# Kernel optimization log

Measured on AMD Instinct MI355X. Metric: run time of the kernel, lower is better.

Reference implementation:

```python
import jax, jax.numpy as jnp
import numpy as np

DIM, HID, E, K = 1024, 2048, 8, 2


def setup_inputs() -> dict:
    key = jax.random.key(0)
    ks = jax.random.split(key, 5)
    x = jax.random.normal(ks[0], (2, 2048, DIM), dtype=jnp.float32)
    # router (torch zero-inits; use small random so routing is non-degenerate)
    router_w = jax.random.normal(ks[1], (DIM, E), dtype=jnp.float32) * 0.02
    router_b = jnp.zeros((E,), dtype=jnp.float32)
    # stacked expert params: w12 [E, dim, 2*hidden], w3 [E, hidden, dim]
    w12 = jax.random.normal(ks[2], (E, DIM, 2 * HID), dtype=jnp.float32) * 0.02
    w3 = jax.random.normal(ks[3], (E, HID, DIM), dtype=jnp.float32) * 0.02
    return {"x": x, "router_w": router_w, "router_b": router_b, "w12": w12, "w3": w3}


def reference(x, router_w, router_b, w12, w3):
    # router logits [b, s, e]; eval mode -> no jitter noise
    logits = jnp.einsum("bsd,de->bse", x, router_w) + router_b
    scores = jax.nn.sigmoid(logits)
    top_v, top_i = jax.lax.top_k(scores, K)            # [b, s, k]
    rw = top_v / (jnp.sum(top_v, axis=-1, keepdims=True) + 1e-6)
    # per-token combine weight for each expert (0 if not routed)
    oh = jax.nn.one_hot(top_i, E, dtype=x.dtype)       # [b, s, k, e]
    cw = jnp.einsum("bsk,bske->bse", rw, oh)           # [b, s, e]
    # dense all-expert SwiGLU (matches original masked-dense math)
    x12 = jnp.einsum("bsd,edh->bseh", x, w12)          # [b, s, e, 2H]
    x1, x2 = jnp.split(x12, 2, axis=-1)
    h = jax.nn.silu(x1) * x2                           # [b, s, e, H]
    eout = jnp.einsum("bseh,ehd->bsed", h, w3)         # [b, s, e, dim]
    out = jnp.einsum("bsed,bse->bsd", eout, cw)
    aux_loss = 0.01 * jnp.mean(logits ** 2)
    return out, aux_loss
```

## Files before the change

kernel.cpp:

```cpp
#include <hip/hip_runtime.h>
#include <hip/hip_bf16.h>
#include <stdint.h>

typedef __bf16 bf16_t;
typedef __bf16 bf16x8 __attribute__((ext_vector_type(8)));
typedef __bf16 bf16x4 __attribute__((ext_vector_type(4)));
typedef float f32x4 __attribute__((ext_vector_type(4)));

#define T_TOK 4096
#define DIM   1024
#define HID   2048
#define NE    8
#define MAXT  72

__device__ __forceinline__ void gload_lds16(const void* g, void* l) {
  __builtin_amdgcn_global_load_lds(
      (const __attribute__((address_space(1))) unsigned int*)g,
      (__attribute__((address_space(3))) unsigned int*)l, 16, 0, 0);
}

__global__ __launch_bounds__(256) void k_wt(const float* __restrict__ in,
                                            bf16_t* __restrict__ out,
                                            int K, int N) {
  __shared__ float tile[128][65];
  const size_t eoff = (size_t)blockIdx.z * K * N;
  const int k0 = blockIdx.y * 128, n0 = blockIdx.x * 64;
  const int tid = threadIdx.x;
#pragma unroll
  for (int it = 0; it < 8; ++it) {
    int k = (tid >> 4) + it * 16;
    int n = (tid & 15) * 4;
    float4 v = *(const float4*)(in + eoff + (size_t)(k0 + k) * N + n0 + n);
    tile[k][n] = v.x; tile[k][n + 1] = v.y; tile[k][n + 2] = v.z; tile[k][n + 3] = v.w;
  }
  __syncthreads();
#pragma unroll
  for (int it = 0; it < 4; ++it) {
    int n = (tid >> 4) + it * 16;
    int kc = (tid & 15) * 8;
    bf16x8 o;
#pragma unroll
    for (int j = 0; j < 8; ++j) o[j] = (bf16_t)tile[kc + j][n];
    *(bf16x8*)(out + eoff + (size_t)(n0 + n) * K + k0 + kc) = o;
  }
}

__global__ __launch_bounds__(256) void k_router(const float* __restrict__ x,
    const float* __restrict__ rw, const float* __restrict__ rb,
    int* __restrict__ counts, int* __restrict__ top_i, float* __restrict__ top_w,
    float* __restrict__ aux, bf16_t* __restrict__ xb) {
  int t = blockIdx.x * 4 + (threadIdx.x >> 6);
  int lane = threadIdx.x & 63;
  const float* xt = x + (size_t)t * DIM;
  float acc[8] = {0.f,0.f,0.f,0.f,0.f,0.f,0.f,0.f};
#pragma unroll
  for (int it = 0; it < 4; ++it) {
    int i = (it * 64 + lane) * 4;
    float4 xv = *(const float4*)(xt + i);
    bf16x4 o;
    o[0] = (bf16_t)xv.x; o[1] = (bf16_t)xv.y; o[2] = (bf16_t)xv.z; o[3] = (bf16_t)xv.w;
    *(bf16x4*)(xb + (size_t)t * DIM + i) = o;
#pragma unroll
    for (int c = 0; c < 4; ++c) {
      float v = (c == 0) ? xv.x : (c == 1) ? xv.y : (c == 2) ? xv.z : xv.w;
      float4 r0 = *(const float4*)(rw + (size_t)(i + c) * 8);
      float4 r1 = *(const float4*)(rw + (size_t)(i + c) * 8 + 4);
      acc[0] += v * r0.x; acc[1] += v * r0.y; acc[2] += v * r0.z; acc[3] += v * r0.w;
      acc[4] += v * r1.x; acc[5] += v * r1.y; acc[6] += v * r1.z; acc[7] += v * r1.w;
    }
  }
#pragma unroll
  for (int m = 32; m >= 1; m >>= 1) {
#pragma unroll
    for (int e = 0; e < 8; ++e) acc[e] += __shfl_xor(acc[e], m, 64);
  }
  if (lane == 0) {
    float s[8]; float sumsq = 0.f;
#pragma unroll
    for (int e = 0; e < 8; ++e) {
      float lg = acc[e] + rb[e];
      sumsq += lg * lg;
      s[e] = 1.f / (1.f + __expf(-lg));
    }
    int i1 = 0;
#pragma unroll
    for (int e = 1; e < 8; ++e) if (s[e] > s[i1]) i1 = e;
    int i2 = (i1 == 0) ? 1 : 0;
#pragma unroll
    for (int e = 0; e < 8; ++e) if (e != i1 && s[e] > s[i2]) i2 = e;
    float v1 = s[i1], v2 = s[i2];
    float den = v1 + v2 + 1e-6f;
    top_i[2 * t]     = i1; top_i[2 * t + 1] = i2;
    top_w[2 * t]     = v1 / den;
    top_w[2 * t + 1] = v2 / den;
    atomicAdd(&counts[i1], 1);
    atomicAdd(&counts[i2], 1);
    atomicAdd(aux, 0.01f * sumsq * (1.f / 32768.f));
  }
}

__global__ void k_plan(const int* __restrict__ counts, int* __restrict__ base,
                       int* __restrict__ tile_e, int* __restrict__ tile_m0) {
  if (threadIdx.x == 0) {
    int s = 0, nt = 0;
    for (int e = 0; e < NE; ++e) {
      base[e] = s;
      int c = counts[e];
      for (int m0 = 0; m0 < c; m0 += 128) { tile_e[nt] = e; tile_m0[nt] = m0; ++nt; }
      s += c;
    }
    for (; nt < MAXT; ++nt) tile_e[nt] = -1;
  }
}

__global__ __launch_bounds__(256) void k_gather(const int* __restrict__ top_i,
    const float* __restrict__ top_w, const int* __restrict__ base,
    int* __restrict__ fill, int* __restrict__ slot_token, float* __restrict__ slot_wt,
    int* __restrict__ slot_of) {
  int t = blockIdx.x * 256 + threadIdx.x;
  if (t >= T_TOK) return;
#pragma unroll
  for (int j = 0; j < 2; ++j) {
    int e = top_i[2 * t + j];
    int p = atomicAdd(&fill[e], 1);
    int g = base[e] + p;
    slot_token[g] = t;
    slot_wt[g]    = top_w[2 * t + j];
    slot_of[2 * t + j] = g;
  }
}

__global__ __launch_bounds__(256) void k_gemm1(
    const bf16_t* __restrict__ xb, const bf16_t* __restrict__ w12t,
    const int* __restrict__ counts, const int* __restrict__ base,
    const int* __restrict__ tile_e, const int* __restrict__ tile_m0,
    const int* __restrict__ slot_token, bf16_t* __restrict__ h) {
  const int e = tile_e[blockIdx.y];
  if (e < 0) return;
  const int m0  = tile_m0[blockIdx.y];
  const int cnt = counts[e];
  const int bas = base[e];
  const int n0  = blockIdx.x * 64;
  const bf16_t* W1 = w12t + (size_t)e * (4096u * 1024u) + (size_t)n0 * 1024u;
  const bf16_t* W2 = W1 + (size_t)2048 * 1024;

  __shared__ bf16_t sA[2][128 * 64];
  __shared__ bf16_t sB1[2][64 * 64];
  __shared__ bf16_t sB2[2][64 * 64];

  const int tid = threadIdx.x, lane = tid & 63, wid = tid >> 6;
  const int wr = wid >> 1, wc = wid & 1;
  const int lr = lane >> 3, sw = (lane & 7) ^ lr;

  int tokA[4];
#pragma unroll
  for (int i = 0; i < 4; ++i) {
    int row = m0 + wid * 32 + i * 8 + lr;
    tokA[i] = slot_token[bas + (row < cnt ? row : cnt - 1)];
  }

  auto stage = [&](int p, int k0) {
#pragma unroll
    for (int i = 0; i < 4; ++i)
      gload_lds16(xb + (size_t)tokA[i] * DIM + k0 + sw * 8,
                  &sA[p][(wid * 32 + i * 8) * 64]);
#pragma unroll
    for (int i = 0; i < 2; ++i) {
      int n = wid * 16 + i * 8 + lr;
      gload_lds16(W1 + (size_t)n * 1024 + k0 + sw * 8, &sB1[p][(wid * 16 + i * 8) * 64]);
      gload_lds16(W2 + (size_t)n * 1024 + k0 + sw * 8, &sB2[p][(wid * 16 + i * 8) * 64]);
    }
  };

  f32x4 acc1[4][2] = {};
  f32x4 acc2[4][2] = {};

  stage(0, 0);
  stage(1, 64);

  const int NT = DIM / 64;
  for (int t = 0; t < NT; ++t) {
    const int p = t & 1;
    if (t + 2 < NT) asm volatile("s_waitcnt vmcnt(8)" ::: "memory");
    else            asm volatile("s_waitcnt vmcnt(0)" ::: "memory");
    __builtin_amdgcn_s_barrier();
    asm volatile("" ::: "memory");
    __builtin_amdgcn_s_setprio(1);
#pragma unroll
    for (int kk = 0; kk < 2; ++kk) {
      const int g = kk * 4 + (lane >> 4);
      bf16x8 a[4], b1[2], b2[2];
#pragma unroll
      for (int mf = 0; mf < 4; ++mf) {
        int r = wr * 64 + mf * 16 + (lane & 15);
        a[mf] = *(const bf16x8*)(&sA[p][r * 64 + ((g ^ (r & 7)) << 3)]);
      }
#pragma unroll
      for (int nf = 0; nf < 2; ++nf) {
        int n = wc * 32 + nf * 16 + (lane & 15);
        b1[nf] = *(const bf16x8*)(&sB1[p][n * 64 + ((g ^ (n & 7)) << 3)]);
        b2[nf] = *(const bf16x8*)(&sB2[p][n * 64 + ((g ^ (n & 7)) << 3)]);
      }
#pragma unroll
      for (int mf = 0; mf < 4; ++mf)
#pragma unroll
        for (int nf = 0; nf < 2; ++nf) {
          acc1[mf][nf] = __builtin_amdgcn_mfma_f32_16x16x32_bf16(a[mf], b1[nf], acc1[mf][nf], 0, 0, 0);
          acc2[mf][nf] = __builtin_amdgcn_mfma_f32_16x16x32_bf16(a[mf], b2[nf], acc2[mf][nf], 0, 0, 0);
        }
    }
    __builtin_amdgcn_s_setprio(0);
    __builtin_amdgcn_sched_barrier(0);
    __builtin_amdgcn_s_barrier();
    asm volatile("" ::: "memory");
    if (t + 2 < NT) stage(p, (t + 2) * 64);
  }

#pragma unroll
  for (int mf = 0; mf < 4; ++mf)
#pragma unroll
    for (int r = 0; r < 4; ++r) {
      int m = wr * 64 + mf * 16 + ((lane >> 4) << 2) + r;
      if (m0 + m < cnt) {
        size_t rowoff = (size_t)(bas + m0 + m) * HID + n0;
#pragma unroll
        for (int nf = 0; nf < 2; ++nf) {
          int col = wc * 32 + nf * 16 + (lane & 15);
          float d1 = acc1[mf][nf][r], d2 = acc2[mf][nf][r];
          h[rowoff + col] = (bf16_t)((d1 / (1.f + __expf(-d1))) * d2);
        }
      }
    }
}

__global__ __launch_bounds__(256) void k_gemm2(
    const bf16_t* __restrict__ h, const bf16_t* __restrict__ w3t,
    const int* __restrict__ counts, const int* __restrict__ base,
    const int* __restrict__ tile_e, const int* __restrict__ tile_m0,
    const float* __restrict__ slot_wt, bf16_t* __restrict__ eout) {
  const int e = tile_e[blockIdx.y];
  if (e < 0) return;
  const int m0  = tile_m0[blockIdx.y];
  const int cnt = counts[e];
  const int bas = base[e];
  const int n0 = blockIdx.x * 128;
  const bf16_t* W = w3t + (size_t)e * (1024u * 2048u);

  __shared__ bf16_t sA[2][128 * 64];
  __shared__ bf16_t sB[2][128 * 64];

  const int tid = threadIdx.x, lane = tid & 63, wid = tid >> 6;
  const int wr = wid >> 1, wc = wid & 1;
  const int lr = lane >> 3, sw = (lane & 7) ^ lr;

  int rowA[4];
#pragma unroll
  for (int i = 0; i < 4; ++i) {
    int row = m0 + wid * 32 + i * 8 + lr;
    rowA[i] = bas + (row < cnt ? row : cnt - 1);
  }

  auto stage = [&](int p, int k0) {
#pragma unroll
    for (int i = 0; i < 4; ++i) {
      int rr = wid * 32 + i * 8;
      gload_lds16(h + (size_t)rowA[i] * HID + k0 + sw * 8, &sA[p][rr * 64]);
      gload_lds16(W + (size_t)(n0 + rr + lr) * 2048 + k0 + sw * 8, &sB[p][rr * 64]);
    }
  };

  f32x4 acc[4][4] = {};

  stage(0, 0);
  stage(1, 64);

  const int NT = HID / 64;
  for (int t = 0; t < NT; ++t) {
    const int p = t & 1;
    if (t + 2 < NT) asm volatile("s_waitcnt vmcnt(8)" ::: "memory");
    else            asm volatile("s_waitcnt vmcnt(0)" ::: "memory");
    __builtin_amdgcn_s_barrier();
    asm volatile("" ::: "memory");
    __builtin_amdgcn_s_setprio(1);
#pragma unroll
    for (int kk = 0; kk < 2; ++kk) {
      const int g = kk * 4 + (lane >> 4);
      bf16x8 a[4], b[4];
#pragma unroll
      for (int mf = 0; mf < 4; ++mf) {
        int r = wr * 64 + mf * 16 + (lane & 15);
        a[mf] = *(const bf16x8*)(&sA[p][r * 64 + ((g ^ (r & 7)) << 3)]);
      }
#pragma unroll
      for (int nf = 0; nf < 4; ++nf) {
        int n = wc * 64 + nf * 16 + (lane & 15);
        b[nf] = *(const bf16x8*)(&sB[p][n * 64 + ((g ^ (n & 7)) << 3)]);
      }
#pragma unroll
      for (int mf = 0; mf < 4; ++mf)
#pragma unroll
        for (int nf = 0; nf < 4; ++nf)
          acc[mf][nf] = __builtin_amdgcn_mfma_f32_16x16x32_bf16(a[mf], b[nf], acc[mf][nf], 0, 0, 0);
    }
    __builtin_amdgcn_s_setprio(0);
    __builtin_amdgcn_sched_barrier(0);
    __builtin_amdgcn_s_barrier();
    asm volatile("" ::: "memory");
    if (t + 2 < NT) stage(p, (t + 2) * 64);
  }

#pragma unroll
  for (int mf = 0; mf < 4; ++mf)
#pragma unroll
    for (int r = 0; r < 4; ++r) {
      int m = wr * 64 + mf * 16 + ((lane >> 4) << 2) + r;
      if (m0 + m < cnt) {
        int gs = bas + m0 + m;
        float wt = slot_wt[gs];
        size_t o = (size_t)gs * DIM + n0;
#pragma unroll
        for (int nf = 0; nf < 4; ++nf) {
          int col = wc * 64 + nf * 16 + (lane & 15);
          eout[o + col] = (bf16_t)(acc[mf][nf][r] * wt);
        }
      }
    }
}

__global__ __launch_bounds__(256) void k_combine(const bf16_t* __restrict__ eout,
    const int* __restrict__ slot_of, float* __restrict__ out) {
  const int t = blockIdx.x;
  const int c = threadIdx.x * 4;
  const int g0 = slot_of[2 * t], g1 = slot_of[2 * t + 1];
  bf16x4 a = *(const bf16x4*)(eout + (size_t)g0 * DIM + c);
  bf16x4 b = *(const bf16x4*)(eout + (size_t)g1 * DIM + c);
  float4 o;
  o.x = (float)a[0] + (float)b[0];
  o.y = (float)a[1] + (float)b[1];
  o.z = (float)a[2] + (float)b[2];
  o.w = (float)a[3] + (float)b[3];
  *(float4*)(out + (size_t)t * DIM + c) = o;
}

extern "C" void kernel_launch(void* const* d_in, const int* in_sizes, int n_in,
                              void* d_out, int out_size, void* d_ws, size_t ws_size,
                              hipStream_t stream) {
  const float* x   = (const float*)d_in[0];
  const float* rw  = (const float*)d_in[1];
  const float* rb  = (const float*)d_in[2];
  const float* w12 = (const float*)d_in[3];
  const float* w3  = (const float*)d_in[4];
  float* out = (float*)d_out;
  float* aux = out + (size_t)T_TOK * DIM;

  char* ws = (char*)d_ws;
  int*   counts     = (int*)(ws + 0);
  int*   fill       = (int*)(ws + 64);
  int*   base       = (int*)(ws + 128);
  int*   top_i      = (int*)(ws + 4096);
  float* top_w      = (float*)(ws + 4096 + 32768);
  int*   slot_token = (int*)(ws + 4096 + 65536);
  float* slot_wt    = (float*)(ws + 4096 + 98304);
  int*   slot_of    = (int*)(ws + 4096 + 131072);
  int*   tile_e     = (int*)(ws + 4096 + 163840);
  int*   tile_m0    = (int*)(ws + 4096 + 164352);
  bf16_t* xb        = (bf16_t*)(ws + 262144);
  bf16_t* h         = (bf16_t*)(ws + 262144 + 8388608);
  bf16_t* wT        = (bf16_t*)(ws + 262144 + 8388608 + 33554432);
  bf16_t* eout      = (bf16_t*)((char*)wT + 33554432);

  hipMemsetAsync(ws, 0, 256, stream);
  hipMemsetAsync(aux, 0, sizeof(float), stream);

  k_wt<<<dim3(64, 8, NE), dim3(256), 0, stream>>>(w12, wT, DIM, 2 * HID);
  k_router<<<dim3(T_TOK / 4), dim3(256), 0, stream>>>(x, rw, rb, counts, top_i, top_w,
                                                      aux, xb);
  k_plan<<<dim3(1), dim3(64), 0, stream>>>(counts, base, tile_e, tile_m0);
  k_gather<<<dim3(T_TOK / 256), dim3(256), 0, stream>>>(top_i, top_w, base, fill,
                                                        slot_token, slot_wt, slot_of);
  k_gemm1<<<dim3(HID / 64, MAXT), dim3(256), 0, stream>>>(
      xb, wT, counts, base, tile_e, tile_m0, slot_token, h);
  k_wt<<<dim3(16, 16, NE), dim3(256), 0, stream>>>(w3, wT, HID, DIM);
  k_gemm2<<<dim3(DIM / 128, MAXT), dim3(256), 0, stream>>>(
      h, wT, counts, base, tile_e, tile_m0, slot_wt, eout);
  k_combine<<<dim3(T_TOK), dim3(256), 0, stream>>>(eout, slot_of, out);
}
```

Before: 383.3 us.

## Replace weight transpose kernels with flat bf16 conversion and LDS transpose reads

Drops the two LDS-tiled fp32→bf16 transpose kernels and uses one grid-stride kernel that converts w12 and w3 to bf16 in their original [K,N] layout. The GEMMs now load B tiles row-major in K and use ds_read_b64_tr_b16 to build the transposed MFMA operands in LDS. This removes the transpose kernel's strided LDS work and one launch. In exchange it adds explicit lgkmcnt waits inside the inner loop and depends on hand-computed transpose-read offsets being correct. eout now aliases the w12c buffer, which is safe only because gemm1 has finished reading it before gemm2 writes.

```diff
diff --git a/kernel.cpp b/kernel.cpp
--- a/kernel.cpp
+++ b/kernel.cpp
@@ -6,6 +6,8 @@
 typedef __bf16 bf16x8 __attribute__((ext_vector_type(8)));
 typedef __bf16 bf16x4 __attribute__((ext_vector_type(4)));
 typedef float f32x4 __attribute__((ext_vector_type(4)));
+typedef uint32_t u32x2 __attribute__((ext_vector_type(2)));
+typedef __attribute__((address_space(3))) const uint8_t* lds3;
 
 #define T_TOK 4096
 #define DIM   1024
@@ -19,29 +21,30 @@
       (__attribute__((address_space(3))) unsigned int*)l, 16, 0, 0);
 }
 
-__global__ __launch_bounds__(256) void k_wt(const float* __restrict__ in,
-                                            bf16_t* __restrict__ out,
-                                            int K, int N) {
-  __shared__ float tile[128][65];
-  const size_t eoff = (size_t)blockIdx.z * K * N;
-  const int k0 = blockIdx.y * 128, n0 = blockIdx.x * 64;
-  const int tid = threadIdx.x;
-#pragma unroll
-  for (int it = 0; it < 8; ++it) {
-    int k = (tid >> 4) + it * 16;
-    int n = (tid & 15) * 4;
-    float4 v = *(const float4*)(in + eoff + (size_t)(k0 + k) * N + n0 + n);
-    tile[k][n] = v.x; tile[k][n + 1] = v.y; tile[k][n + 2] = v.z; tile[k][n + 3] = v.w;
-  }
-  __syncthreads();
-#pragma unroll
-  for (int it = 0; it < 4; ++it) {
-    int n = (tid >> 4) + it * 16;
-    int kc = (tid & 15) * 8;
-    bf16x8 o;
-#pragma unroll
-    for (int j = 0; j < 8; ++j) o[j] = (bf16_t)tile[kc + j][n];
-    *(bf16x8*)(out + eoff + (size_t)(n0 + n) * K + k0 + kc) = o;
+#define TRR(dst, a, OFF) \
+  asm volatile("ds_read_b64_tr_b16 %0, %1 offset:" OFF : "=v"(dst) : "v"(a))
+
+__device__ __forceinline__ bf16x8 mk8(u32x2 lo, u32x2 hi) {
+  uint4 t; t.x = lo[0]; t.y = lo[1]; t.z = hi[0]; t.w = hi[1];
+  return __builtin_bit_cast(bf16x8, t);
+}
+
+__global__ __launch_bounds__(256) void k_conv(const float* __restrict__ w12,
+    const float* __restrict__ w3, bf16_t* __restrict__ w12c, bf16_t* __restrict__ w3c) {
+  const size_t N12 = 33554432ull;
+  const size_t NT  = 50331648ull;
+  const size_t stride = (size_t)gridDim.x * 256 * 4;
+  for (size_t i = ((size_t)blockIdx.x * 256 + threadIdx.x) * 4; i < NT; i += stride) {
+    if (i < N12) {
+      float4 v = *(const float4*)(w12 + i);
+      bf16x4 o; o[0]=(bf16_t)v.x; o[1]=(bf16_t)v.y; o[2]=(bf16_t)v.z; o[3]=(bf16_t)v.w;
+      *(bf16x4*)(w12c + i) = o;
+    } else {
+      size_t j = i - N12;
+      float4 v = *(const float4*)(w3 + j);
+      bf16x4 o; o[0]=(bf16_t)v.x; o[1]=(bf16_t)v.y; o[2]=(bf16_t)v.z; o[3]=(bf16_t)v.w;
+      *(bf16x4*)(w3c + j) = o;
+    }
   }
 }
 
@@ -131,7 +134,7 @@
 }
 
 __global__ __launch_bounds__(256) void k_gemm1(
-    const bf16_t* __restrict__ xb, const bf16_t* __restrict__ w12t,
+    const bf16_t* __restrict__ xb, const bf16_t* __restrict__ w12c,
     const int* __restrict__ counts, const int* __restrict__ base,
     const int* __restrict__ tile_e, const int* __restrict__ tile_m0,
     const int* __restrict__ slot_token, bf16_t* __restrict__ h) {
@@ -141,8 +144,8 @@
   const int cnt = counts[e];
   const int bas = base[e];
   const int n0  = blockIdx.x * 64;
-  const bf16_t* W1 = w12t + (size_t)e * (4096u * 1024u) + (size_t)n0 * 1024u;
-  const bf16_t* W2 = W1 + (size_t)2048 * 1024;
+  const bf16_t* W1 = w12c + (size_t)e * (1024u * 4096u) + n0;
+  const bf16_t* W2 = W1 + 2048;
 
   __shared__ bf16_t sA[2][128 * 64];
   __shared__ bf16_t sB1[2][64 * 64];
@@ -159,18 +162,26 @@
     tokA[i] = slot_token[bas + (row < cnt ? row : cnt - 1)];
   }
 
+  int brow0, bcol0, brow1, bcol1;
+  { int b = tid >> 3, w = tid & 7;
+    brow0 = ((b >> 2) << 2) + (w >> 1); bcol0 = (b & 3) * 16 + (w & 1) * 8; }
+  { int g2 = 256 + tid; int b = g2 >> 3, w = g2 & 7;
+    brow1 = ((b >> 2) << 2) + (w >> 1); bcol1 = (b & 3) * 16 + (w & 1) * 8; }
+
   auto stage = [&](int p, int k0) {
 #pragma unroll
     for (int i = 0; i < 4; ++i)
       gload_lds16(xb + (size_t)tokA[i] * DIM + k0 + sw * 8,
                   &sA[p][(wid * 32 + i * 8) * 64]);
-#pragma unroll
-    for (int i = 0; i < 2; ++i) {
-      int n = wid * 16 + i * 8 + lr;
-      gload_lds16(W1 + (size_t)n * 1024 + k0 + sw * 8, &sB1[p][(wid * 16 + i * 8) * 64]);
-      gload_lds16(W2 + (size_t)n * 1024 + k0 + sw * 8, &sB2[p][(wid * 16 + i * 8) * 64]);
-    }
+    gload_lds16(W1 + (size_t)(k0 + brow0) * 4096 + bcol0, &sB1[p][tid * 8]);
+    gload_lds16(W1 + (size_t)(k0 + brow1) * 4096 + bcol1, &sB1[p][2048 + tid * 8]);
+    gload_lds16(W2 + (size_t)(k0 + brow0) * 4096 + bcol0, &sB2[p][tid * 8]);
+    gload_lds16(W2 + (size_t)(k0 + brow1) * 4096 + bcol1, &sB2[p][2048 + tid * 8]);
   };
+
+  const int trOff = (lane >> 4) * 1024 + wc * 256 + (lane & 15) * 8;
+  lds3 bB1 = (lds3)(const uint8_t*)&sB1[0][0];
+  lds3 bB2 = (lds3)(const uint8_t*)&sB2[0][0];
 
   f32x4 acc1[4][2] = {};
   f32x4 acc2[4][2] = {};
@@ -189,24 +200,29 @@
 #pragma unroll
     for (int kk = 0; kk < 2; ++kk) {
       const int g = kk * 4 + (lane >> 4);
-      bf16x8 a[4], b1[2], b2[2];
+      bf16x8 a[4];
 #pragma unroll
       for (int mf = 0; mf < 4; ++mf) {
         int r = wr * 64 + mf * 16 + (lane & 15);
         a[mf] = *(const bf16x8*)(&sA[p][r * 64 + ((g ^ (r & 7)) << 3)]);
       }
-#pragma unroll
-      for (int nf = 0; nf < 2; ++nf) {
-        int n = wc * 32 + nf * 16 + (lane & 15);
-        b1[nf] = *(const bf16x8*)(&sB1[p][n * 64 + ((g ^ (n & 7)) << 3)]);
-        b2[nf] = *(const bf16x8*)(&sB2[p][n * 64 + ((g ^ (n & 7)) << 3)]);
-      }
+      lds3 a1 = bB1 + p * 8192 + kk * 4096 + trOff;
+      lds3 a2 = bB2 + p * 8192 + kk * 4096 + trOff;
+      u32x2 q0, q1, q2, q3, s0, s1, s2, s3;
+      TRR(q0, a1, "0");   TRR(q1, a1, "512");
+      TRR(q2, a1, "128"); TRR(q3, a1, "640");
+      TRR(s0, a2, "0");   TRR(s1, a2, "512");
+      TRR(s2, a2, "128"); TRR(s3, a2, "640");
+      asm volatile("s_waitcnt lgkmcnt(0)" ::: "memory");
+      __builtin_amdgcn_sched_barrier(0);
+      bf16x8 b1f[2] = { mk8(q0, q1), mk8(q2, q3) };
+      bf16x8 b2f[2] = { mk8(s0, s1), mk8(s2, s3) };
 #pragma unroll
       for (int mf = 0; mf < 4; ++mf)
 #pragma unroll
         for (int nf = 0; nf < 2; ++nf) {
-          acc1[mf][nf] = __builtin_amdgcn_mfma_f32_16x16x32_bf16(a[mf], b1[nf], acc1[mf][nf], 0, 0, 0);
-          acc2[mf][nf] = __builtin_amdgcn_mfma_f32_16x16x32_bf16(a[mf], b2[nf], acc2[mf][nf], 0, 0, 0);
+          acc1[mf][nf] = __builtin_amdgcn_mfma_f32_16x16x32_bf16(a[mf], b1f[nf], acc1[mf][nf], 0, 0, 0);
+          acc2[mf][nf] = __builtin_amdgcn_mfma_f32_16x16x32_bf16(a[mf], b2f[nf], acc2[mf][nf], 0, 0, 0);
         }
     }
     __builtin_amdgcn_s_setprio(0);
@@ -234,7 +250,7 @@
 }
 
 __global__ __launch_bounds__(256) void k_gemm2(
-    const bf16_t* __restrict__ h, const bf16_t* __restrict__ w3t,
+    const bf16_t* __restrict__ h, const bf16_t* __restrict__ w3c,
     const int* __restrict__ counts, const int* __restrict__ base,
     const int* __restrict__ tile_e, const int* __restrict__ tile_m0,
     const float* __restrict__ slot_wt, bf16_t* __restrict__ eout) {
@@ -244,7 +260,7 @@
   const int cnt = counts[e];
   const int bas = base[e];
   const int n0 = blockIdx.x * 128;
-  const bf16_t* W = w3t + (size_t)e * (1024u * 2048u);
+  const bf16_t* W = w3c + (size_t)e * (2048u * 1024u) + n0;
 
   __shared__ bf16_t sA[2][128 * 64];
   __shared__ bf16_t sB[2][128 * 64];
@@ -260,14 +276,28 @@
     rowA[i] = bas + (row < cnt ? row : cnt - 1);
   }
 
+  int br[4], bc[4];
+#pragma unroll
+  for (int j = 0; j < 4; ++j) {
+    int g = j * 256 + tid;
+    int b = g >> 3, w = g & 7;
+    br[j] = ((b >> 3) << 2) + (w >> 1);
+    bc[j] = (b & 7) * 16 + (w & 1) * 8;
+  }
+
   auto stage = [&](int p, int k0) {
 #pragma unroll
-    for (int i = 0; i < 4; ++i) {
-      int rr = wid * 32 + i * 8;
-      gload_lds16(h + (size_t)rowA[i] * HID + k0 + sw * 8, &sA[p][rr * 64]);
-      gload_lds16(W + (size_t)(n0 + rr + lr) * 2048 + k0 + sw * 8, &sB[p][rr * 64]);
-    }
+    for (int i = 0; i < 4; ++i)
+      gload_lds16(h + (size_t)rowA[i] * HID + k0 + sw * 8,
+                  &sA[p][(wid * 32 + i * 8) * 64]);
+#pragma unroll
+    for (int j = 0; j < 4; ++j)
+      gload_lds16(W + (size_t)(k0 + br[j]) * 1024 + bc[j],
+                  &sB[p][(j * 256 + tid) * 8]);
   };
+
+  const int trOff = (lane >> 4) * 2048 + wc * 512 + (lane & 15) * 8;
+  lds3 bB = (lds3)(const uint8_t*)&sB[0][0];
 
   f32x4 acc[4][4] = {};
 
@@ -285,22 +315,26 @@
 #pragma unroll
     for (int kk = 0; kk < 2; ++kk) {
       const int g = kk * 4 + (lane >> 4);
-      bf16x8 a[4], b[4];
+      bf16x8 a[4];
 #pragma unroll
       for (int mf = 0; mf < 4; ++mf) {
         int r = wr * 64 + mf * 16 + (lane & 15);
         a[mf] = *(const bf16x8*)(&sA[p][r * 64 + ((g ^ (r & 7)) << 3)]);
       }
-#pragma unroll
-      for (int nf = 0; nf < 4; ++nf) {
-        int n = wc * 64 + nf * 16 + (lane & 15);
-        b[nf] = *(const bf16x8*)(&sB[p][n * 64 + ((g ^ (n & 7)) << 3)]);
-      }
+      lds3 ab = bB + p * 16384 + kk * 8192 + trOff;
+      u32x2 q0, q1, q2, q3, q4, q5, q6, q7;
+      TRR(q0, ab, "0");   TRR(q1, ab, "1024");
+      TRR(q2, ab, "128"); TRR(q3, ab, "1152");
+      TRR(q4, ab, "256"); TRR(q5, ab, "1280");
+      TRR(q6, ab, "384"); TRR(q7, ab, "1408");
+      asm volatile("s_waitcnt lgkmcnt(0)" ::: "memory");
+      __builtin_amdgcn_sched_barrier(0);
+      bf16x8 bf[4] = { mk8(q0, q1), mk8(q2, q3), mk8(q4, q5), mk8(q6, q7) };
 #pragma unroll
       for (int mf = 0; mf < 4; ++mf)
 #pragma unroll
         for (int nf = 0; nf < 4; ++nf)
-          acc[mf][nf] = __builtin_amdgcn_mfma_f32_16x16x32_bf16(a[mf], b[nf], acc[mf][nf], 0, 0, 0);
+          acc[mf][nf] = __builtin_amdgcn_mfma_f32_16x16x32_bf16(a[mf], bf[nf], acc[mf][nf], 0, 0, 0);
     }
     __builtin_amdgcn_s_setprio(0);
     __builtin_amdgcn_sched_barrier(0);
@@ -366,22 +400,22 @@
   int*   tile_m0    = (int*)(ws + 4096 + 164352);
   bf16_t* xb        = (bf16_t*)(ws + 262144);
   bf16_t* h         = (bf16_t*)(ws + 262144 + 8388608);
-  bf16_t* wT        = (bf16_t*)(ws + 262144 + 8388608 + 33554432);
-  bf16_t* eout      = (bf16_t*)((char*)wT + 33554432);
+  bf16_t* w12c      = (bf16_t*)(ws + 262144 + 8388608 + 33554432);
+  bf16_t* w3c       = (bf16_t*)((char*)w12c + 67108864);
+  bf16_t* eout      = w12c;
 
   hipMemsetAsync(ws, 0, 256, stream);
   hipMemsetAsync(aux, 0, sizeof(float), stream);
 
-  k_wt<<<dim3(64, 8, NE), dim3(256), 0, stream>>>(w12, wT, DIM, 2 * HID);
+  k_conv<<<dim3(2048), dim3(256), 0, stream>>>(w12, w3, w12c, w3c);
   k_router<<<dim3(T_TOK / 4), dim3(256), 0, stream>>>(x, rw, rb, counts, top_i, top_w,
                                                       aux, xb);
   k_plan<<<dim3(1), dim3(64), 0, stream>>>(counts, base, tile_e, tile_m0);
   k_gather<<<dim3(T_TOK / 256), dim3(256), 0, stream>>>(top_i, top_w, base, fill,
                                                         slot_token, slot_wt, slot_of);
   k_gemm1<<<dim3(HID / 64, MAXT), dim3(256), 0, stream>>>(
-      xb, wT, counts, base, tile_e, tile_m0, slot_token, h);
-  k_wt<<<dim3(16, 16, NE), dim3(256), 0, stream>>>(w3, wT, HID, DIM);
+      xb, w12c, counts, base, tile_e, tile_m0, slot_token, h);
   k_gemm2<<<dim3(DIM / 128, MAXT), dim3(256), 0, stream>>>(
-      h, wT, counts, base, tile_e, tile_m0, slot_wt, eout);
+      h, w3c, counts, base, tile_e, tile_m0, slot_wt, eout);
   k_combine<<<dim3(T_TOK), dim3(256), 0, stream>>>(eout, slot_of, out);
 }
```

Result: no change. 386.0 us (+0.7%).
